# Kernel optimization log

Measured on AMD Instinct MI355X. Metric: run time of the kernel, lower is better.

The kernel has to match this reference:

```python
import jax, jax.numpy as jnp
import numpy as np

EMB = 1024
HEADS = 8
HEAD_DIM = EMB // HEADS


def setup_inputs() -> dict:
    key = jax.random.key(0)
    ks = jax.random.split(key, 11)
    B, S = 4, 2048
    scale = 1.0 / np.sqrt(EMB)
    inp = {
        "query": jax.random.normal(ks[0], (B, S, EMB), jnp.float32),
        "key": jax.random.normal(ks[1], (B, S, EMB), jnp.float32),
        "value": jax.random.normal(ks[2], (B, S, EMB), jnp.float32),
        "Wq": jax.random.normal(ks[3], (EMB, EMB), jnp.float32) * scale,
        "bq": jnp.zeros((EMB,), jnp.float32),
        "Wk": jax.random.normal(ks[4], (EMB, EMB), jnp.float32) * scale,
        "bk": jnp.zeros((EMB,), jnp.float32),
        "Wv": jax.random.normal(ks[5], (EMB, EMB), jnp.float32) * scale,
        "bv": jnp.zeros((EMB,), jnp.float32),
        "Wo": jax.random.normal(ks[6], (EMB, EMB), jnp.float32) * scale,
        "bo": jnp.zeros((EMB,), jnp.float32),
    }
    return inp


def _split_heads(x):
    B, S, _ = x.shape
    return x.reshape(B, S, HEADS, HEAD_DIM).transpose(0, 2, 1, 3)  # [B,H,S,D]


def reference(query, key, value, Wq, bq, Wk, bk, Wv, bv, Wo, bo):
    Q = _split_heads(query @ Wq.T + bq)
    K = _split_heads(key @ Wk.T + bk)
    V = _split_heads(value @ Wv.T + bv)
    # [B,H,S,S] attention scores, scaled by sqrt(head_dim)
    scores = jnp.einsum("bhqd,bhkd->bhqk", Q, K) / jnp.sqrt(
        jnp.asarray(HEAD_DIM, Q.dtype)
    )
    attention = jax.nn.softmax(scores, axis=-1)
    # dropout is identity in eval mode
    x = jnp.einsum("bhqk,bhkd->bhqd", attention, V)
    B, H, S, D = x.shape
    x = x.transpose(0, 2, 1, 3).reshape(B, S, EMB)
    x = x @ Wo.T + bo
    return (x, attention)
```

## Files before the change

### kernel.cpp

```cpp
#include <hip/hip_runtime.h>
#include <hip/hip_bf16.h>
#include <math.h>

#define BB 4
#define SS 2048
#define EMB 1024
#define HH 8
#define DD 128

typedef __attribute__((ext_vector_type(8))) short bf16x8;
typedef __attribute__((ext_vector_type(4))) float f32x4;
typedef __attribute__((ext_vector_type(2))) unsigned int u32x2;

__device__ __forceinline__ unsigned short f2bf(float f) {
    unsigned u = __builtin_bit_cast(unsigned, f);
    u += 0x7FFFu + ((u >> 16) & 1u);
    return (unsigned short)(u >> 16);
}

__device__ __forceinline__ void gload_lds16(const void* g, void* l) {
    __builtin_amdgcn_global_load_lds(
        (const __attribute__((address_space(1))) unsigned int*)g,
        (__attribute__((address_space(3))) unsigned int*)l, 16, 0, 0);
}

#define SB0 __builtin_amdgcn_sched_barrier(0)

__global__ void f2bf3_kernel(const float* __restrict__ a, const float* __restrict__ b,
                             const float* __restrict__ c, unsigned short* __restrict__ dst,
                             int n4) {
    const float* src = blockIdx.z == 0 ? a : (blockIdx.z == 1 ? b : c);
    unsigned short* d = dst + (size_t)blockIdx.z * ((size_t)n4 * 4);
    int i = blockIdx.x * blockDim.x + threadIdx.x;
    int stride = gridDim.x * blockDim.x;
    for (; i < n4; i += stride) {
        float4 f = ((const float4*)src)[i];
        ushort4 o;
        o.x = f2bf(f.x); o.y = f2bf(f.y); o.z = f2bf(f.z); o.w = f2bf(f.w);
        ((ushort4*)d)[i] = o;
    }
}

__global__ void f2bf4_kernel(const float* __restrict__ a, const float* __restrict__ b,
                             const float* __restrict__ c, const float* __restrict__ e,
                             unsigned short* __restrict__ dst, int n4) {
    const float* src = blockIdx.z == 0 ? a : (blockIdx.z == 1 ? b : (blockIdx.z == 2 ? c : e));
    unsigned short* d = dst + (size_t)blockIdx.z * ((size_t)n4 * 4);
    int i = blockIdx.x * blockDim.x + threadIdx.x;
    int stride = gridDim.x * blockDim.x;
    for (; i < n4; i += stride) {
        float4 f = ((const float4*)src)[i];
        ushort4 o;
        o.x = f2bf(f.x); o.y = f2bf(f.y); o.z = f2bf(f.z); o.w = f2bf(f.w);
        ((ushort4*)d)[i] = o;
    }
}

template <int MODE>
__device__ __forceinline__ void gemm_core(const unsigned short* __restrict__ A,
                                          const unsigned short* __restrict__ Bw,
                                          const float* __restrict__ bias,
                                          void* __restrict__ Cout, float scale)
{
    __shared__ short As[2][128 * 32];
    __shared__ short Bs[2][128 * 32];
    const int K = 1024;
    const int m0 = blockIdx.x * 128, n0 = blockIdx.y * 128;
    const int t = threadIdx.x;
    const int lane = t & 63, w = t >> 6;
    const int wr = w >> 1, wc = w & 1;
    const int g = lane >> 4, li = lane & 15;
    f32x4 acc[4][4] = {};

    auto stage = [&](int k0, int buf) {
        #pragma unroll
        for (int i = 0; i < 2; ++i) {
            int idx = i * 256 + t;
            int row = idx >> 2, col = (idx & 3) * 8;
            gload_lds16(A  + (size_t)(m0 + row) * K + k0 + col, &As[buf][idx * 8]);
            gload_lds16(Bw + (size_t)(n0 + row) * K + k0 + col, &Bs[buf][idx * 8]);
        }
    };

    stage(0, 0);
    for (int ki = 0; ki < 32; ++ki) {
        const int cur = ki & 1;
        if (ki < 31) {
            stage((ki + 1) * 32, cur ^ 1);
            asm volatile("s_waitcnt vmcnt(4)" ::: "memory");
        } else {
            asm volatile("s_waitcnt vmcnt(0)" ::: "memory");
        }
        SB0; __builtin_amdgcn_s_barrier(); SB0;

        bf16x8 af[4], bfr[4];
        #pragma unroll
        for (int mi = 0; mi < 4; ++mi)
            af[mi] = *(const bf16x8*)&As[cur][(wr * 64 + mi * 16 + li) * 32 + g * 8];
        #pragma unroll
        for (int ni = 0; ni < 4; ++ni)
            bfr[ni] = *(const bf16x8*)&Bs[cur][(wc * 64 + ni * 16 + li) * 32 + g * 8];
        #pragma unroll
        for (int mi = 0; mi < 4; ++mi) {
            #pragma unroll
            for (int ni = 0; ni < 4; ++ni)
                acc[mi][ni] = __builtin_amdgcn_mfma_f32_16x16x32_bf16(
                    af[mi], bfr[ni], acc[mi][ni], 0, 0, 0);
        }
        asm volatile("s_waitcnt lgkmcnt(0)" ::: "memory");
        SB0; __builtin_amdgcn_s_barrier(); SB0;
    }

    #pragma unroll
    for (int mi = 0; mi < 4; ++mi) {
        #pragma unroll
        for (int ni = 0; ni < 4; ++ni) {
            int n = n0 + wc * 64 + ni * 16 + li;
            float bv = bias[n];
            #pragma unroll
            for (int i = 0; i < 4; ++i) {
                int m = m0 + wr * 64 + mi * 16 + g * 4 + i;
                float v = acc[mi][ni][i] + bv;
                if (MODE == 0) {
                    v *= scale;
                    int b = m >> 11, s = m & 2047, h = n >> 7, d = n & 127;
                    ((unsigned short*)Cout)[((((size_t)b * HH + h) * SS + s) << 7) + d] = f2bf(v);
                } else {
                    ((float*)Cout)[(size_t)m * EMB + n] = v;
                }
            }
        }
    }
}

__global__ __launch_bounds__(256, 2)
void gemm_qkv(const unsigned short* __restrict__ XB, const unsigned short* __restrict__ WB,
              const float* __restrict__ bq, const float* __restrict__ bk,
              const float* __restrict__ bv, unsigned short* __restrict__ QKVb, float qscale)
{
    const size_t NX = (size_t)BB * SS * EMB;
    const size_t NW = (size_t)EMB * EMB;
    const int z = blockIdx.z;
    const float* bias = z == 0 ? bq : (z == 1 ? bk : bv);
    gemm_core<0>(XB + z * NX, WB + z * NW, bias, QKVb + z * NX, z == 0 ? qscale : 1.f);
}

__global__ __launch_bounds__(256, 2)
void gemm_out(const unsigned short* __restrict__ Ob, const unsigned short* __restrict__ Wo,
              const float* __restrict__ bo, float* __restrict__ outx)
{
    gemm_core<1>(Ob, Wo, bo, outx, 1.f);
}

__global__ __launch_bounds__(256, 2)
void attn_kernel(const unsigned short* __restrict__ Qb,
                 const unsigned short* __restrict__ Kb,
                 const unsigned short* __restrict__ Vb,
                 float* __restrict__ attn,
                 unsigned short* __restrict__ Ob)
{
    __shared__ short Ks[64 * 128];
    __shared__ short Vt[128 * 64];
    __shared__ short Ps[4][16 * 72];

    const int t = threadIdx.x;
    const int lane = t & 63, w = t >> 6;
    const int g = lane >> 4, li = lane & 15;
    const int bh = blockIdx.y;
    const int q0 = blockIdx.x * 64 + w * 16;

    const unsigned short* Kbh = Kb + (size_t)bh * SS * DD;
    const unsigned short* Vbh = Vb + (size_t)bh * SS * DD;

    bf16x8 qf[4];
    {
        const unsigned short* qp = Qb + ((size_t)bh * SS + q0 + li) * DD + g * 8;
        #pragma unroll
        for (int kk = 0; kk < 4; ++kk) qf[kk] = *(const bf16x8*)(qp + kk * 32);
    }

    float lacc = 0.f;

    auto stageK = [&](int kt2, char* dst) {
        const char* ksrc = (const char*)(Kbh + kt2 * 64 * DD);
        #pragma unroll
        for (int i = 0; i < 4; ++i) {
            int lb = (i * 256 + t) * 16;
            int row = lb >> 8;
            gload_lds16(ksrc + (lb ^ ((row & 7) << 4)), dst + lb);
        }
    };

    stageK(0, (char*)Ks);
    for (int kt = 0; kt < 32; ++kt) {
        const char* cur = (kt & 1) ? (const char*)Vt : (const char*)Ks;
        char* nxt = (kt & 1) ? (char*)Ks : (char*)Vt;
        if (kt < 31) {
            stageK(kt + 1, nxt);
            asm volatile("s_waitcnt vmcnt(4)" ::: "memory");
        } else {
            asm volatile("s_waitcnt vmcnt(0)" ::: "memory");
        }
        SB0; __builtin_amdgcn_s_barrier(); SB0;

        #pragma unroll
        for (int kc = 0; kc < 4; ++kc) {
            f32x4 a = {0.f, 0.f, 0.f, 0.f};
            int row = kc * 16 + li;
            int sw = (row & 7) << 4;
            #pragma unroll
            for (int kk = 0; kk < 4; ++kk) {
                bf16x8 kf = *(const bf16x8*)(cur + row * 256 + ((kk * 64 + g * 16) ^ sw));
                a = __builtin_amdgcn_mfma_f32_16x16x32_bf16(kf, qf[kk], a, 0, 0, 0);
            }
            lacc += __builtin_amdgcn_exp2f(a[0]) + __builtin_amdgcn_exp2f(a[1])
                  + __builtin_amdgcn_exp2f(a[2]) + __builtin_amdgcn_exp2f(a[3]);
        }
        __builtin_amdgcn_s_barrier(); SB0;
    }

    float ts = lacc;
    ts += __shfl_xor(ts, 16, 64);
    ts += __shfl_xor(ts, 32, 64);
    const float rl = 1.f / ts;

    f32x4 O[8] = {};
    float* arow = attn + (size_t)bh * SS * SS;

    bf16x8 va[2], vbr[2];
    #pragma unroll
    for (int i = 0; i < 2; ++i) {
        int idx = i * 256 + t;
        int k0 = (idx >> 4) * 2, d0 = (idx & 15) * 8;
        va[i]  = *(const bf16x8*)(Vbh + k0 * DD + d0);
        vbr[i] = *(const bf16x8*)(Vbh + (k0 + 1) * DD + d0);
    }

    for (int kt = 0; kt < 32; ++kt) {
        __syncthreads();
        const char* ksrc = (const char*)(Kbh + kt * 64 * DD);
        #pragma unroll
        for (int i = 0; i < 4; ++i) {
            int lb = (i * 256 + t) * 16;
            int row = lb >> 8;
            gload_lds16(ksrc + (lb ^ ((row & 7) << 4)), (char*)Ks + lb);
        }
        #pragma unroll
        for (int i = 0; i < 2; ++i) {
            int idx = i * 256 + t;
            int kpair = idx >> 4, d0 = (idx & 15) * 8;
            #pragma unroll
            for (int j = 0; j < 8; ++j) {
                unsigned pk = (unsigned)(unsigned short)va[i][j]
                            | ((unsigned)(unsigned short)vbr[i][j] << 16);
                int d = d0 + j;
                int ba = (d * 128 + kpair * 4) ^ (((d >> 3) & 7) << 4);
                *(unsigned*)((char*)Vt + ba) = pk;
            }
        }
        __syncthreads();

        if (kt < 31) {
            const unsigned short* vn = Vbh + (kt + 1) * 64 * DD;
            #pragma unroll
            for (int i = 0; i < 2; ++i) {
                int idx = i * 256 + t;
                int k0 = (idx >> 4) * 2, d0 = (idx & 15) * 8;
                va[i]  = *(const bf16x8*)(vn + k0 * DD + d0);
                vbr[i] = *(const bf16x8*)(vn + (k0 + 1) * DD + d0);
            }
        }

        #pragma unroll
        for (int kc = 0; kc < 4; ++kc) {
            f32x4 a = {0.f, 0.f, 0.f, 0.f};
            int row = kc * 16 + li;
            int sw = (row & 7) << 4;
            #pragma unroll
            for (int kk = 0; kk < 4; ++kk) {
                bf16x8 kf = *(const bf16x8*)((const char*)Ks + row * 256 + ((kk * 64 + g * 16) ^ sw));
                a = __builtin_amdgcn_mfma_f32_16x16x32_bf16(kf, qf[kk], a, 0, 0, 0);
            }
            float p0 = __builtin_amdgcn_exp2f(a[0]) * rl;
            float p1 = __builtin_amdgcn_exp2f(a[1]) * rl;
            float p2 = __builtin_amdgcn_exp2f(a[2]) * rl;
            float p3 = __builtin_amdgcn_exp2f(a[3]) * rl;
            f32x4 pv = {p0, p1, p2, p3};
            __builtin_nontemporal_store(pv,
                (f32x4*)(arow + (size_t)(q0 + li) * SS + kt * 64 + kc * 16 + g * 4));
            unsigned pk0, pk1;
            asm("v_cvt_pk_bf16_f32 %0, %1, %2" : "=v"(pk0) : "v"(p0), "v"(p1));
            asm("v_cvt_pk_bf16_f32 %0, %1, %2" : "=v"(pk1) : "v"(p2), "v"(p3));
            u32x2 pw = {pk0, pk1};
            *(u32x2*)((char*)&Ps[w][0] + li * 144 + kc * 32 + g * 8) = pw;
        }
        asm volatile("s_waitcnt lgkmcnt(0)" ::: "memory");
        SB0;

        bf16x8 pf0 = *(const bf16x8*)((const char*)&Ps[w][0] + li * 144 + g * 16);
        bf16x8 pf1 = *(const bf16x8*)((const char*)&Ps[w][0] + li * 144 + 64 + g * 16);
        #pragma unroll
        for (int dt = 0; dt < 8; ++dt) {
            int dr = dt * 16 + li;
            int vsw = ((dr >> 3) & 7) << 4;
            bf16x8 vf0 = *(const bf16x8*)((const char*)Vt + dr * 128 + ((g * 16) ^ vsw));
            bf16x8 vf1 = *(const bf16x8*)((const char*)Vt + dr * 128 + ((64 + g * 16) ^ vsw));
            O[dt] = __builtin_amdgcn_mfma_f32_16x16x32_bf16(pf0, vf0, O[dt], 0, 0, 0);
            O[dt] = __builtin_amdgcn_mfma_f32_16x16x32_bf16(pf1, vf1, O[dt], 0, 0, 0);
        }
    }

    const int b = bh >> 3, h = bh & 7;
    #pragma unroll
    for (int dt = 0; dt < 8; ++dt) {
        #pragma unroll
        for (int i = 0; i < 4; ++i) {
            size_t r = (size_t)b * SS + q0 + g * 4 + i;
            Ob[r * EMB + h * DD + dt * 16 + li] = f2bf(O[dt][i]);
        }
    }
}

extern "C" void kernel_launch(void* const* d_in, const int* in_sizes, int n_in,
                              void* d_out, int out_size, void* d_ws, size_t ws_size,
                              hipStream_t stream)
{
    const float* q  = (const float*)d_in[0];
    const float* k  = (const float*)d_in[1];
    const float* v  = (const float*)d_in[2];
    const float* Wq = (const float*)d_in[3];
    const float* bq = (const float*)d_in[4];
    const float* Wk = (const float*)d_in[5];
    const float* bk = (const float*)d_in[6];
    const float* Wv = (const float*)d_in[7];
    const float* bv = (const float*)d_in[8];
    const float* Wo = (const float*)d_in[9];
    const float* bo = (const float*)d_in[10];

    const size_t NX = (size_t)BB * SS * EMB;
    const size_t NW = (size_t)EMB * EMB;

    unsigned short* Qb = (unsigned short*)d_ws;
    unsigned short* Ob = Qb + 3 * NX;
    unsigned short* WB = Ob + NX;

    float* outx = (float*)d_out;
    float* attn = outx + NX;
    unsigned short* XB = (unsigned short*)attn;

    f2bf3_kernel<<<dim3(1024, 1, 3), 256, 0, stream>>>(q, k, v, XB, (int)(NX / 4));
    f2bf4_kernel<<<dim3(128, 1, 4), 256, 0, stream>>>(Wq, Wk, Wv, Wo, WB, (int)(NW / 4));

    const float qscale = 1.4426950408889634f / sqrtf((float)DD);
    gemm_qkv<<<dim3(64, 8, 3), 256, 0, stream>>>(XB, WB, bq, bk, bv, Qb, qscale);

    attn_kernel<<<dim3(32, 32), 256, 0, stream>>>(Qb, Qb + NX, Qb + 2 * NX, attn, Ob);

    gemm_out<<<dim3(64, 8), 256, 0, stream>>>(Ob, WB + 3 * NW, bo, outx);
}
```

Measured before the change: 355.3 us.

## Register-prefetch K/V two tiles ahead and remap block-to-head assignment

The attention loop now loads K and V tiles into registers two iterations ahead and writes them to LDS after the consumers of the previous tile finish, replacing the direct global-to-LDS K load and the full-block syncs with s_barrier plus lgkmcnt waits. Block indices are also remapped so that consecutive hardware block ids spread across batch-head pairs in a swizzled order, which is meant to improve L2 and cache locality of K/V across XCDs. Overlapping the global loads with compute should hide memory latency. In exchange it raises register pressure and makes the barrier ordering more delicate.

```diff
diff --git a/kernel.cpp b/kernel.cpp
--- a/kernel.cpp
+++ b/kernel.cpp
@@ -166,8 +166,11 @@
     const int t = threadIdx.x;
     const int lane = t & 63, w = t >> 6;
     const int g = lane >> 4, li = lane & 15;
-    const int bh = blockIdx.y;
-    const int q0 = blockIdx.x * 64 + w * 16;
+
+    const int hwid = blockIdx.x + (blockIdx.y << 5);
+    const int idx = hwid >> 3;
+    const int bh = (hwid & 7) * 4 + (idx & 3);
+    const int q0 = (idx >> 2) * 64 + w * 16;
 
     const unsigned short* Kbh = Kb + (size_t)bh * SS * DD;
     const unsigned short* Vbh = Vb + (size_t)bh * SS * DD;
@@ -227,28 +230,38 @@
     f32x4 O[8] = {};
     float* arow = attn + (size_t)bh * SS * SS;
 
+    bf16x8 ka[4];
     bf16x8 va[2], vbr[2];
-    #pragma unroll
-    for (int i = 0; i < 2; ++i) {
-        int idx = i * 256 + t;
-        int k0 = (idx >> 4) * 2, d0 = (idx & 15) * 8;
-        va[i]  = *(const bf16x8*)(Vbh + k0 * DD + d0);
-        vbr[i] = *(const bf16x8*)(Vbh + (k0 + 1) * DD + d0);
-    }
-
-    for (int kt = 0; kt < 32; ++kt) {
-        __syncthreads();
-        const char* ksrc = (const char*)(Kbh + kt * 64 * DD);
+
+    auto issueK = [&](int kt2) {
+        const unsigned short* kn = Kbh + kt2 * 64 * DD;
+        #pragma unroll
+        for (int i = 0; i < 4; ++i)
+            ka[i] = *(const bf16x8*)(kn + (size_t)(i * 256 + t) * 8);
+    };
+    auto writeK = [&]() {
         #pragma unroll
         for (int i = 0; i < 4; ++i) {
             int lb = (i * 256 + t) * 16;
             int row = lb >> 8;
-            gload_lds16(ksrc + (lb ^ ((row & 7) << 4)), (char*)Ks + lb);
-        }
+            *(bf16x8*)((char*)Ks + (lb ^ ((row & 7) << 4))) = ka[i];
+        }
+    };
+    auto issueV = [&](int kt2) {
+        const unsigned short* vn = Vbh + kt2 * 64 * DD;
         #pragma unroll
         for (int i = 0; i < 2; ++i) {
-            int idx = i * 256 + t;
-            int kpair = idx >> 4, d0 = (idx & 15) * 8;
+            int idx2 = i * 256 + t;
+            int k0 = (idx2 >> 4) * 2, d0 = (idx2 & 15) * 8;
+            va[i]  = *(const bf16x8*)(vn + k0 * DD + d0);
+            vbr[i] = *(const bf16x8*)(vn + (k0 + 1) * DD + d0);
+        }
+    };
+    auto scatterV = [&]() {
+        #pragma unroll
+        for (int i = 0; i < 2; ++i) {
+            int idx2 = i * 256 + t;
+            int kpair = idx2 >> 4, d0 = (idx2 & 15) * 8;
             #pragma unroll
             for (int j = 0; j < 8; ++j) {
                 unsigned pk = (unsigned)(unsigned short)va[i][j]
@@ -258,19 +271,15 @@
                 *(unsigned*)((char*)Vt + ba) = pk;
             }
         }
-        __syncthreads();
-
-        if (kt < 31) {
-            const unsigned short* vn = Vbh + (kt + 1) * 64 * DD;
-            #pragma unroll
-            for (int i = 0; i < 2; ++i) {
-                int idx = i * 256 + t;
-                int k0 = (idx >> 4) * 2, d0 = (idx & 15) * 8;
-                va[i]  = *(const bf16x8*)(vn + k0 * DD + d0);
-                vbr[i] = *(const bf16x8*)(vn + (k0 + 1) * DD + d0);
-            }
-        }
-
+    };
+
+    issueK(0); issueV(0);
+    writeK(); scatterV();
+    issueK(1); issueV(1);
+    asm volatile("s_waitcnt lgkmcnt(0)" ::: "memory");
+    SB0; __builtin_amdgcn_s_barrier(); SB0;
+
+    for (int kt = 0; kt < 32; ++kt) {
         #pragma unroll
         for (int kc = 0; kc < 4; ++kc) {
             f32x4 a = {0.f, 0.f, 0.f, 0.f};
@@ -296,9 +305,12 @@
         }
         asm volatile("s_waitcnt lgkmcnt(0)" ::: "memory");
         SB0;
-
         bf16x8 pf0 = *(const bf16x8*)((const char*)&Ps[w][0] + li * 144 + g * 16);
         bf16x8 pf1 = *(const bf16x8*)((const char*)&Ps[w][0] + li * 144 + 64 + g * 16);
+
+        SB0; __builtin_amdgcn_s_barrier(); SB0;
+        if (kt < 31) writeK();
+
         #pragma unroll
         for (int dt = 0; dt < 8; ++dt) {
             int dr = dt * 16 + li;
@@ -308,6 +320,10 @@
             O[dt] = __builtin_amdgcn_mfma_f32_16x16x32_bf16(pf0, vf0, O[dt], 0, 0, 0);
             O[dt] = __builtin_amdgcn_mfma_f32_16x16x32_bf16(pf1, vf1, O[dt], 0, 0, 0);
         }
+        asm volatile("s_waitcnt lgkmcnt(0)" ::: "memory");
+        SB0; __builtin_amdgcn_s_barrier(); SB0;
+        if (kt < 31) scatterV();
+        if (kt < 30) { issueK(kt + 2); issueV(kt + 2); }
     }
 
     const int b = bh >> 3, h = bh & 7;
```

Measured after the change: 395.0 us. +11.2%, slower.
